# Optimization experiments

Measured on AMD Instinct MI355X. Metric: run time of the kernel, lower is better.

## Reference

```python
import jax, jax.numpy as jnp
import numpy as np

B, H, L, D = 2, 16, 1024, 64
LMAX = 2048  # max_sequence_length: patterns built & normalized at LMAX, then sliced to L
PI = float(np.pi)


def _scale_pattern(freq):
    # pattern[h, t, d] = exp(i(t+ph)) + exp(i(2t+ph)) + exp(i(0.5t+ph)), ph = 2*pi*h/H
    # identical across d, so keep [H, L, 1] and broadcast over D
    phase = 2.0 * PI * jnp.arange(H, dtype=jnp.float32) / H          # [H]
    t = jnp.linspace(0.0, 2.0 * PI * freq, LMAX)                     # [LMAX]
    a1 = t[None, :] + phase[:, None]
    a2 = 2.0 * t[None, :] + phase[:, None]
    a3 = 0.5 * t[None, :] + phase[:, None]
    pr = jnp.cos(a1) + jnp.cos(a2) + jnp.cos(a3)                     # [H, LMAX]
    pi_ = jnp.sin(a1) + jnp.sin(a2) + jnp.sin(a3)
    norm = jnp.sqrt(jnp.sum(pr * pr + pi_ * pi_, axis=1, keepdims=True))  # over full LMAX
    pr, pi_ = pr / norm, pi_ / norm
    return pr[:, :L, None], pi_[:, :L, None]                          # [H, L, 1]


def _expert_total_pattern():
    # 8 experts x 3 aspects; pattern[t, d] = exp(i(f*t + 2*pi*d/D)), normalized per
    # column over LMAX (|exp|=1 -> norm sqrt(LMAX)). Elementwise complex multiply is
    # linear, so the expert stage equals x * sum(all patterns)/(sqrt(3)*sqrt(8)).
    freqs = np.array([[0.3 + 0.1 * i, 0.2 + 0.1 * i, 0.1 + 0.1 * i]
                      for i in range(8)], dtype=np.float32).reshape(-1)   # [24]
    t = jnp.linspace(0.0, 2.0 * PI, LMAX)                                 # [LMAX]
    phase_d = 2.0 * PI * jnp.arange(D, dtype=jnp.float32) / D             # [D]
    ang = jnp.asarray(freqs)[:, None, None] * t[None, :, None] + phase_d[None, None, :]  # [24, LMAX, D]
    col_norm = 1.0 / np.sqrt(float(LMAX))
    denom = np.sqrt(3.0) * np.sqrt(8.0)
    pr = jnp.sum(jnp.cos(ang), axis=0) * (col_norm / denom)               # [LMAX, D]
    pi_ = jnp.sum(jnp.sin(ang), axis=0) * (col_norm / denom)
    return pr[:L], pi_[:L]                                                # [L, D]


def _process_scale(Qr, Qi, Kr, Ki, Vr, Vi, pr, pi_):
    # complex elementwise pattern multiply
    Qpr = Qr * pr - Qi * pi_
    Qpi = Qr * pi_ + Qi * pr
    Kpr = Kr * pr - Ki * pi_
    Kpi = Kr * pi_ + Ki * pr
    # complex scores = Qp @ Kp^T (no conjugation, matching the torch code)
    sr = jnp.einsum('bhld,bhmd->bhlm', Qpr, Kpr) - jnp.einsum('bhld,bhmd->bhlm', Qpi, Kpi)
    si = jnp.einsum('bhld,bhmd->bhlm', Qpr, Kpi) + jnp.einsum('bhld,bhmd->bhlm', Qpi, Kpr)
    mag = jnp.sqrt(sr * sr + si * si) / np.sqrt(float(D))
    w = jax.nn.softmax(mag, axis=-1)
    return (jnp.einsum('bhlm,bhmd->bhld', w, Vr),
            jnp.einsum('bhlm,bhmd->bhld', w, Vi))


def reference(Q_real, Q_imag, K_real, K_imag, V_real, V_imag):
    scale_freqs = [1.0, 0.5, 0.25, 0.1]  # char, word, phrase, sentence
    acc_r = jnp.zeros_like(Q_real)
    acc_i = jnp.zeros_like(Q_real)
    for f in scale_freqs:
        pr, pi_ = _scale_pattern(f)
        o_r, o_i = _process_scale(Q_real, Q_imag, K_real, K_imag, V_real, V_imag, pr, pi_)
        acc_r = acc_r + o_r
        acc_i = acc_i + o_i
    inv = 1.0 / np.sqrt(float(len(scale_freqs)))
    acc_r = acc_r * inv
    acc_i = acc_i * inv
    # expert mixing (linear in x -> single fused complex elementwise multiply)
    epr, epi = _expert_total_pattern()  # [L, D], broadcast over B,H
    out_r = acc_r * epr - acc_i * epi
    out_i = acc_r * epi + acc_i * epr
    return jnp.stack([out_r, out_i], axis=0)  # [2, B, H, L, D] (real, imag)


def setup_inputs() -> dict:
    key = jax.random.key(0)
    ks = jax.random.split(key, 6)
    shape = (B, H, L, D)
    names = ['Q_real', 'Q_imag', 'K_real', 'K_imag', 'V_real', 'V_imag']
    return {n: jax.random.normal(k, shape, dtype=jnp.float32) for n, k in zip(names, ks)}
```

## Files before the change

### kernel.cpp

```cpp
#include <hip/hip_runtime.h>
#include <math.h>

typedef short bf16x8 __attribute__((ext_vector_type(8)));
typedef float f32x4 __attribute__((ext_vector_type(4)));

#define BDIM 256
constexpr int B_ = 2, H_ = 16, L_ = 1024, D_ = 64, LMAX_ = 2048;
constexpr int BH_ = B_ * H_;
constexpr float PI_F = 3.14159265358979323846f;

constexpr int WS_SVP = 0;
constexpr int WS_KBR = 65536;
constexpr int WS_KBI = WS_KBR + 1048576;
constexpr int WS_VTR = WS_KBI + 1048576;
constexpr int WS_VTI = WS_VTR + 1048576;

__device__ __forceinline__ unsigned short f2b(float x) {
    union { float f; unsigned u; } v; v.f = x;
    return (unsigned short)((v.u + 0x8000u) >> 16);
}
__device__ __forceinline__ unsigned pk2(float a, float b) {
    union { float f; unsigned u; } va, vb; va.f = a; vb.f = b;
    return ((va.u + 0x8000u) >> 16) | ((vb.u + 0x8000u) & 0xFFFF0000u);
}
__device__ __forceinline__ uint4 pack4(const float4& a, const float4& b) {
    return make_uint4(pk2(a.x, a.y), pk2(a.z, a.w), pk2(b.x, b.y), pk2(b.z, b.w));
}

#define MFMA(a, b, c) __builtin_amdgcn_mfma_f32_16x16x32_bf16((a), (b), (c), 0, 0, 0)

__device__ __forceinline__ float a_val(int s, int l, float4 invn) {
    const float fr = (s == 0) ? 1.0f : (s == 1) ? 0.5f : (s == 2) ? 0.25f : 0.1f;
    const float iv = (s == 0) ? invn.x : (s == 1) ? invn.y : (s == 2) ? invn.z : invn.w;
    float t = (2.0f * PI_F * fr / (float)(LMAX_ - 1)) * (float)l;
    float m2 = 3.0f + 2.0f * cosf(t) + 2.0f * cosf(0.5f * t) + 2.0f * cosf(1.5f * t);
    return sqrtf(fmaxf(m2, 0.0f)) * iv;
}

__global__ __launch_bounds__(BDIM)
void prep_kernel(const float* __restrict__ Kr, const float* __restrict__ Ki,
                 const float* __restrict__ Vr, const float* __restrict__ Vi,
                 float* __restrict__ ws) {
    const int tid = threadIdx.x;
    const int blk = blockIdx.x;
    unsigned short* KbR = (unsigned short*)(ws + WS_KBR);
    unsigned short* KbI = (unsigned short*)(ws + WS_KBI);
    unsigned short* VtR = (unsigned short*)(ws + WS_VTR);
    unsigned short* VtI = (unsigned short*)(ws + WS_VTI);

    if (blk < 256) {
        const int comp = blk >> 7;
        const float* src = comp ? Ki : Kr;
        unsigned short* dst = comp ? KbI : KbR;
        size_t b0 = (size_t)(blk & 127) * 16384;
#pragma unroll
        for (int i = 0; i < 4; ++i) {
            size_t e = b0 + (size_t)(i * 256 + tid) * 16;
            float4 x0 = *(const float4*)(src + e);
            float4 x1 = *(const float4*)(src + e + 4);
            float4 x2 = *(const float4*)(src + e + 8);
            float4 x3 = *(const float4*)(src + e + 12);
            *(uint4*)(dst + e) = pack4(x0, x1);
            *(uint4*)(dst + e + 8) = pack4(x2, x3);
        }
    } else {
        __shared__ unsigned short sT[64 * 70];
        __shared__ float sRed[4 * 64];
        const int vb = blk - 256;
        const int comp = vb & 1, mt = (vb >> 1) & 15, bh = vb >> 5;
        const int m0 = mt * 64;
        const float* src = (comp ? Vi : Vr) + (size_t)bh * 65536 + (size_t)m0 * 64;
        unsigned short* dstA = (comp ? VtI : VtR) + (size_t)bh * 65536;
#pragma unroll
        for (int i = 0; i < 4; ++i) {
            int e = i * 256 + tid;
            int m = e >> 4, d4 = (e & 15) * 4;
            float4 x = *(const float4*)(src + (size_t)m * 64 + d4);
            *(uint2*)&sT[m * 70 + d4] = make_uint2(pk2(x.x, x.y), pk2(x.z, x.w));
        }
        {
            int d = tid & 63, grp = tid >> 6;
            float s = 0.0f;
#pragma unroll
            for (int k = 0; k < 16; ++k) s += src[(size_t)(grp * 16 + k) * 64 + d];
            sRed[grp * 64 + d] = s;
        }
        __syncthreads();
        {
            int d = tid >> 2, ms = (tid & 3) * 16;
            unsigned short v[16];
#pragma unroll
            for (int k = 0; k < 16; ++k) v[k] = sT[(ms + k) * 70 + d];
            unsigned short* dst = dstA + (size_t)d * 1024 + m0 + ms;
            *(uint4*)dst = make_uint4((unsigned)v[0] | ((unsigned)v[1] << 16),
                                      (unsigned)v[2] | ((unsigned)v[3] << 16),
                                      (unsigned)v[4] | ((unsigned)v[5] << 16),
                                      (unsigned)v[6] | ((unsigned)v[7] << 16));
            *(uint4*)(dst + 8) = make_uint4((unsigned)v[8] | ((unsigned)v[9] << 16),
                                            (unsigned)v[10] | ((unsigned)v[11] << 16),
                                            (unsigned)v[12] | ((unsigned)v[13] << 16),
                                            (unsigned)v[14] | ((unsigned)v[15] << 16));
        }
        if (tid < 64)
            ws[WS_SVP + comp * 32768 + bh * 1024 + mt * 64 + tid] =
                sRed[tid] + sRed[64 + tid] + sRed[128 + tid] + sRed[192 + tid];
    }
}

__device__ __forceinline__ void stage64s(const unsigned short* g0, int stride,
                                         unsigned short* lds, int w, int lane) {
#pragma unroll
    for (int i = 0; i < 2; ++i) {
        int c = w * 2 + i;
        int lrow = c * 8 + (lane >> 3);
        int lg = (lane & 7) ^ (lrow & 7);
        const unsigned short* src = g0 + (size_t)lrow * stride + lg * 8;
        __builtin_amdgcn_global_load_lds(
            (const __attribute__((address_space(1))) void*)src,
            (__attribute__((address_space(3))) void*)(lds + c * 512), 16, 0, 0);
    }
}
__device__ __forceinline__ bf16x8 ldfrag(const unsigned short* b, int row, int g) {
    return *(const bf16x8*)&b[row * 64 + ((g ^ (row & 7)) << 3)];
}

__global__ __launch_bounds__(BDIM, 2)
void attn_kernel(const float* __restrict__ Qr, const float* __restrict__ Qi,
                 const float* __restrict__ ws, float* __restrict__ out, float4 invn) {
    __shared__ unsigned short sK0[2][4096], sK1[2][4096];
    __shared__ unsigned short sV0[4096], sV1[4096];
    __shared__ unsigned short sE[4096];
    __shared__ unsigned short sMg[4096];
    __shared__ unsigned short sAmb[4 * 1032];
    __shared__ float sDen[4 * 64];

    const int tid = threadIdx.x;
    const int lane = tid & 63;
    const int w = tid >> 6;
    const int lo16 = lane & 15;
    const int quad = lane >> 4;
    const int blk = blockIdx.x;
    const int bh = (blk & 7) * 4 + (blk >> 7);
    const int qt = (blk >> 3) & 15;
    const int l0 = qt * 64;
    const size_t base = (size_t)bh * (L_ * D_);

    const unsigned short* gKr = (const unsigned short*)(ws + WS_KBR) + (size_t)bh * 65536;
    const unsigned short* gKi = (const unsigned short*)(ws + WS_KBI) + (size_t)bh * 65536;
    const unsigned short* gVr = (const unsigned short*)(ws + WS_VTR) + (size_t)bh * 65536;
    const unsigned short* gVi = (const unsigned short*)(ws + WS_VTI) + (size_t)bh * 65536;

    stage64s(gKr, 64, sK0[0], w, lane);
    stage64s(gKi, 64, sK1[0], w, lane);

    for (int e = tid; e < 4096; e += BDIM) {
        int s = e >> 10, l = e & 1023;
        sAmb[s * 1032 + l] = f2b(a_val(s, l, invn) * 0.125f);
    }

    bf16x8 fQr0, fQr1, fQi0, fQi1, fnQi0, fnQi1;
    {
        const int ql = l0 + w * 16 + lo16;
        const float* qr = Qr + base + (size_t)ql * 64;
        const float* qi = Qi + base + (size_t)ql * 64;
        float4 a0 = *(const float4*)(qr + quad * 8);
        float4 a1 = *(const float4*)(qr + quad * 8 + 4);
        float4 b0 = *(const float4*)(qr + 32 + quad * 8);
        float4 b1 = *(const float4*)(qr + 32 + quad * 8 + 4);
        *(uint4*)&fQr0 = pack4(a0, a1);
        *(uint4*)&fQr1 = pack4(b0, b1);
        a0 = *(const float4*)(qi + quad * 8);
        a1 = *(const float4*)(qi + quad * 8 + 4);
        b0 = *(const float4*)(qi + 32 + quad * 8);
        b1 = *(const float4*)(qi + 32 + quad * 8 + 4);
        *(uint4*)&fQi0 = pack4(a0, a1);
        *(uint4*)&fQi1 = pack4(b0, b1);
        uint4 t0 = *(uint4*)&fQi0, t1 = *(uint4*)&fQi1;
        t0.x ^= 0x80008000u; t0.y ^= 0x80008000u; t0.z ^= 0x80008000u; t0.w ^= 0x80008000u;
        t1.x ^= 0x80008000u; t1.y ^= 0x80008000u; t1.z ^= 0x80008000u; t1.w ^= 0x80008000u;
        *(uint4*)&fnQi0 = t0; *(uint4*)&fnQi1 = t1;
    }

    bf16x8 uf1a = (bf16x8){0, 0, 0, 0, 0, 0, 0, 0};
    uf1a[0] = (short)f2b(a_val(quad, l0 + w * 16 + lo16, invn) * (1.0f / 1024.0f));

    f32x4 accM1 = (f32x4){0.f, 0.f, 0.f, 0.f};
    f32x4 aOutR[4], aOutI[4];
#pragma unroll
    for (int dt = 0; dt < 4; ++dt) {
        aOutR[dt] = (f32x4){0.f, 0.f, 0.f, 0.f};
        aOutI[dt] = (f32x4){0.f, 0.f, 0.f, 0.f};
    }

    __syncthreads();

    int cur = 0;
#pragma unroll 1
    for (int mt = 0; mt < 16; ++mt) {
        const int m0 = mt * 64;
        stage64s(gVr + m0, 1024, sV0, w, lane);
        stage64s(gVi + m0, 1024, sV1, w, lane);
        if (mt < 15) {
            stage64s(gKr + (size_t)(m0 + 64) * 64, 64, sK0[cur ^ 1], w, lane);
            stage64s(gKi + (size_t)(m0 + 64) * 64, 64, sK1[cur ^ 1], w, lane);
        }
        const unsigned short* cK0 = sK0[cur];
        const unsigned short* cK1 = sK1[cur];

#pragma unroll
        for (int ct = 0; ct < 4; ++ct) {
            const int mrow = ct * 16 + lo16;
            bf16x8 kr0 = ldfrag(cK0, mrow, quad), kr1 = ldfrag(cK0, mrow, quad + 4);
            bf16x8 ki0 = ldfrag(cK1, mrow, quad), ki1 = ldfrag(cK1, mrow, quad + 4);
            f32x4 aR = (f32x4){0.f, 0.f, 0.f, 0.f};
            f32x4 aI = (f32x4){0.f, 0.f, 0.f, 0.f};
            __builtin_amdgcn_s_setprio(1);
            aR = MFMA(kr0, fQr0, aR);  aR = MFMA(kr1, fQr1, aR);
            aR = MFMA(ki0, fnQi0, aR); aR = MFMA(ki1, fnQi1, aR);
            aI = MFMA(ki0, fQr0, aI);  aI = MFMA(ki1, fQr1, aI);
            aI = MFMA(kr0, fQi0, aI);  aI = MFMA(kr1, fQi1, aI);
            __builtin_amdgcn_s_setprio(0);
            float mg0 = sqrtf(fmaf(aR[0], aR[0], aI[0] * aI[0]));
            float mg1 = sqrtf(fmaf(aR[1], aR[1], aI[1] * aI[1]));
            float mg2 = sqrtf(fmaf(aR[2], aR[2], aI[2] * aI[2]));
            float mg3 = sqrtf(fmaf(aR[3], aR[3], aI[3] * aI[3]));
            bf16x8 bf1 = (bf16x8){0, 0, 0, 0, 0, 0, 0, 0};
            bf1[0] = (short)sAmb[quad * 1032 + m0 + ct * 16 + lo16];
            f32x4 z = (f32x4){0.f, 0.f, 0.f, 0.f};
            f32x4 a1 = MFMA(bf1, uf1a, z);
            float p0 = mg0 * a1[0], p1 = mg1 * a1[1];
            float p2 = mg2 * a1[2], p3 = mg3 * a1[3];
            int l = w * 16 + lo16;
            int gph = (ct * 2 + (quad >> 1)) ^ (l & 7);
            *(uint2*)&sE[l * 64 + gph * 8 + (quad & 1) * 4] =
                make_uint2(pk2(p0, p1), pk2(p2, p3));
            *(uint2*)&sMg[l * 64 + gph * 8 + (quad & 1) * 4] =
                make_uint2(pk2(mg0, mg1), pk2(mg2, mg3));
        }
        {
            bf16x8 mf0 = ldfrag(sMg, w * 16 + lo16, quad);
            bf16x8 mf1 = ldfrag(sMg, w * 16 + lo16, quad + 4);
            bf16x8 b0 = (bf16x8){0, 0, 0, 0, 0, 0, 0, 0};
            bf16x8 b1 = (bf16x8){0, 0, 0, 0, 0, 0, 0, 0};
            if (lo16 < 4) {
                b0 = *(const bf16x8*)&sAmb[lo16 * 1032 + m0 + quad * 8];
                b1 = *(const bf16x8*)&sAmb[lo16 * 1032 + m0 + 32 + quad * 8];
            }
            accM1 = MFMA(mf0, b0, accM1);
            accM1 = MFMA(mf1, b1, accM1);
        }
        if (mt < 15) {
            asm volatile("s_waitcnt vmcnt(4)" ::: "memory");
        } else {
            asm volatile("s_waitcnt vmcnt(0)" ::: "memory");
        }
        __builtin_amdgcn_s_barrier();
        {
            bf16x8 pa0 = ldfrag(sE, w * 16 + lo16, quad);
            bf16x8 pa1 = ldfrag(sE, w * 16 + lo16, quad + 4);
            __builtin_amdgcn_s_setprio(1);
#pragma unroll
            for (int dt = 0; dt < 4; ++dt) {
                int dr = dt * 16 + lo16;
                bf16x8 vr0 = ldfrag(sV0, dr, quad), vr1 = ldfrag(sV0, dr, quad + 4);
                bf16x8 vi0 = ldfrag(sV1, dr, quad), vi1 = ldfrag(sV1, dr, quad + 4);
                aOutR[dt] = MFMA(pa0, vr0, aOutR[dt]);
                aOutR[dt] = MFMA(pa1, vr1, aOutR[dt]);
                aOutI[dt] = MFMA(pa0, vi0, aOutI[dt]);
                aOutI[dt] = MFMA(pa1, vi1, aOutI[dt]);
            }
            __builtin_amdgcn_s_setprio(0);
        }
        asm volatile("s_waitcnt vmcnt(0)" ::: "memory");
        __builtin_amdgcn_s_barrier();
        cur ^= 1;
    }

    if (lo16 < 4) {
#pragma unroll
        for (int reg = 0; reg < 4; ++reg) {
            int r = w * 16 + quad * 4 + reg;
            float alv = a_val(lo16, l0 + r, invn);
            sDen[lo16 * 64 + r] = 1.0f / (1024.0f + alv * accM1[reg]);
        }
    }
    float cden[4];
#pragma unroll
    for (int reg = 0; reg < 4; ++reg) {
        int r = w * 16 + quad * 4 + reg;
        cden[reg] = sDen[r] + sDen[64 + r] + sDen[128 + r] + sDen[192 + r];
    }

    const float cE = rsqrtf(2048.0f) * rsqrtf(24.0f);
    float eRr[4], eRi[4];
#pragma unroll
    for (int reg = 0; reg < 4; ++reg) {
        int lrow = l0 + w * 16 + quad * 4 + reg;
        float tl = (2.0f * PI_F / (float)(LMAX_ - 1)) * (float)lrow;
        float s1, c1;
        __sincosf(0.1f * tl, &s1, &c1);
        const float W[10] = {1.f, 2.f, 3.f, 3.f, 3.f, 3.f, 3.f, 3.f, 2.f, 1.f};
        float cr = c1, ci = s1;
        float er = W[0] * cr, ei = W[0] * ci;
#pragma unroll
        for (int k = 1; k < 10; ++k) {
            float nr = cr * c1 - ci * s1;
            float ni = cr * s1 + ci * c1;
            cr = nr; ci = ni;
            er = fmaf(W[k], cr, er);
            ei = fmaf(W[k], ci, ei);
        }
        eRr[reg] = er * cE;
        eRi[reg] = ei * cE;
    }

    const size_t ooff = (size_t)BH_ * L_ * D_;
#pragma unroll
    for (int dt = 0; dt < 4; ++dt) {
        int d = dt * 16 + lo16;
        float svr = 0.0f, svi = 0.0f;
#pragma unroll
        for (int q = 0; q < 16; ++q) {
            svr += ws[WS_SVP + bh * 1024 + q * 64 + d];
            svi += ws[WS_SVP + 32768 + bh * 1024 + q * 64 + d];
        }
        float sp, cp;
        __sincosf((2.0f * PI_F / 64.0f) * (float)d, &sp, &cp);
#pragma unroll
        for (int reg = 0; reg < 4; ++reg) {
            int lrow = l0 + w * 16 + quad * 4 + reg;
            float numR = fmaf(cden[reg], svr, aOutR[dt][reg]) * 0.5f;
            float numI = fmaf(cden[reg], svi, aOutI[dt][reg]) * 0.5f;
            float epr = cp * eRr[reg] - sp * eRi[reg];
            float epi = sp * eRr[reg] + cp * eRi[reg];
            size_t o = base + (size_t)lrow * 64 + d;
            out[o] = numR * epr - numI * epi;
            out[o + ooff] = numR * epi + numI * epr;
        }
    }
}

extern "C" void kernel_launch(void* const* d_in, const int* in_sizes, int n_in,
                              void* d_out, int out_size, void* d_ws, size_t ws_size,
                              hipStream_t stream) {
    const float* Qr = (const float*)d_in[0];
    const float* Qi = (const float*)d_in[1];
    const float* Kr = (const float*)d_in[2];
    const float* Ki = (const float*)d_in[3];
    const float* Vr = (const float*)d_in[4];
    const float* Vi = (const float*)d_in[5];
    float* ws = (float*)d_ws;
    float* out = (float*)d_out;

    const double fr[4] = {1.0, 0.5, 0.25, 0.1};
    float inv[4];
    for (int s = 0; s < 4; ++s) {
        double a = 2.0 * 3.14159265358979323846 * fr[s] / (double)(LMAX_ - 1);
        double S = 3.0 * LMAX_;
        const double mul[3] = {1.0, 0.5, 1.5};
        for (int k = 0; k < 3; ++k) {
            double x = a * mul[k];
            S += 2.0 * (cos(x * 1023.5) * sin(x * 1024.0) / sin(x * 0.5));
        }
        inv[s] = (float)(1.0 / sqrt(S));
    }
    float4 invn = make_float4(inv[0], inv[1], inv[2], inv[3]);

    prep_kernel<<<1280, BDIM, 0, stream>>>(Kr, Ki, Vr, Vi, ws);
    attn_kernel<<<512, BDIM, 0, stream>>>(Qr, Qi, ws, out, invn);
}
```

Measured before the change: 152.2 us.

## Use hardware bf16 pack and sqrt, reuse staged amplitudes, vectorize partial-sum reads

Several micro-optimizations land together. Software bf16 rounding is replaced with the v_cvt_pk_bf16_f32 instruction and sqrtf with raw v_sqrt_f32. The per-row amplitude is now read from the shared-memory table sAmb instead of being recomputed with cosf calls, which needs the barrier moved earlier. The prep kernel writes partial sums transposed so the epilogue can read them with float4 loads instead of 32 strided scalar loads. Raw v_sqrt_f32 drops the precise sqrt correction sequence, and the amplitude now comes from bf16-stored values rather than fp32, so precision may shift slightly.

```diff
diff --git a/kernel.cpp b/kernel.cpp
--- a/kernel.cpp
+++ b/kernel.cpp
@@ -19,12 +19,26 @@
     union { float f; unsigned u; } v; v.f = x;
     return (unsigned short)((v.u + 0x8000u) >> 16);
 }
+__device__ __forceinline__ float b2f(unsigned short x) {
+    union { unsigned u; float f; } v; v.u = ((unsigned)x) << 16;
+    return v.f;
+}
 __device__ __forceinline__ unsigned pk2(float a, float b) {
     union { float f; unsigned u; } va, vb; va.f = a; vb.f = b;
     return ((va.u + 0x8000u) >> 16) | ((vb.u + 0x8000u) & 0xFFFF0000u);
 }
 __device__ __forceinline__ uint4 pack4(const float4& a, const float4& b) {
     return make_uint4(pk2(a.x, a.y), pk2(a.z, a.w), pk2(b.x, b.y), pk2(b.z, b.w));
+}
+__device__ __forceinline__ unsigned cvtpk(float lo, float hi) {
+    unsigned r;
+    asm("v_cvt_pk_bf16_f32 %0, %1, %2" : "=v"(r) : "v"(lo), "v"(hi));
+    return r;
+}
+__device__ __forceinline__ float vsqrt(float x) {
+    float r;
+    asm("v_sqrt_f32 %0, %1" : "=v"(r) : "v"(x));
+    return r;
 }
 
 #define MFMA(a, b, c) __builtin_amdgcn_mfma_f32_16x16x32_bf16((a), (b), (c), 0, 0, 0)
@@ -102,7 +116,7 @@
                                             (unsigned)v[14] | ((unsigned)v[15] << 16));
         }
         if (tid < 64)
-            ws[WS_SVP + comp * 32768 + bh * 1024 + mt * 64 + tid] =
+            ws[WS_SVP + comp * 32768 + bh * 1024 + tid * 16 + mt] =
                 sRed[tid] + sRed[64 + tid] + sRed[128 + tid] + sRed[192 + tid];
     }
 }
@@ -181,8 +195,11 @@
         *(uint4*)&fnQi0 = t0; *(uint4*)&fnQi1 = t1;
     }
 
+    __syncthreads();
+
     bf16x8 uf1a = (bf16x8){0, 0, 0, 0, 0, 0, 0, 0};
-    uf1a[0] = (short)f2b(a_val(quad, l0 + w * 16 + lo16, invn) * (1.0f / 1024.0f));
+    uf1a[0] = (short)f2b(b2f(sAmb[quad * 1032 + (l0 + w * 16 + lo16)]) *
+                         (1.0f / 128.0f));
 
     f32x4 accM1 = (f32x4){0.f, 0.f, 0.f, 0.f};
     f32x4 aOutR[4], aOutI[4];
@@ -192,12 +209,10 @@
         aOutI[dt] = (f32x4){0.f, 0.f, 0.f, 0.f};
     }
 
-    __syncthreads();
-
-    int cur = 0;
 #pragma unroll 1
     for (int mt = 0; mt < 16; ++mt) {
         const int m0 = mt * 64;
+        const int cur = mt & 1;
         stage64s(gVr + m0, 1024, sV0, w, lane);
         stage64s(gVi + m0, 1024, sV1, w, lane);
         if (mt < 15) {
@@ -220,10 +235,10 @@
             aI = MFMA(ki0, fQr0, aI);  aI = MFMA(ki1, fQr1, aI);
             aI = MFMA(kr0, fQi0, aI);  aI = MFMA(kr1, fQi1, aI);
             __builtin_amdgcn_s_setprio(0);
-            float mg0 = sqrtf(fmaf(aR[0], aR[0], aI[0] * aI[0]));
-            float mg1 = sqrtf(fmaf(aR[1], aR[1], aI[1] * aI[1]));
-            float mg2 = sqrtf(fmaf(aR[2], aR[2], aI[2] * aI[2]));
-            float mg3 = sqrtf(fmaf(aR[3], aR[3], aI[3] * aI[3]));
+            float mg0 = vsqrt(fmaf(aR[0], aR[0], aI[0] * aI[0]));
+            float mg1 = vsqrt(fmaf(aR[1], aR[1], aI[1] * aI[1]));
+            float mg2 = vsqrt(fmaf(aR[2], aR[2], aI[2] * aI[2]));
+            float mg3 = vsqrt(fmaf(aR[3], aR[3], aI[3] * aI[3]));
             bf16x8 bf1 = (bf16x8){0, 0, 0, 0, 0, 0, 0, 0};
             bf1[0] = (short)sAmb[quad * 1032 + m0 + ct * 16 + lo16];
             f32x4 z = (f32x4){0.f, 0.f, 0.f, 0.f};
@@ -233,9 +248,9 @@
             int l = w * 16 + lo16;
             int gph = (ct * 2 + (quad >> 1)) ^ (l & 7);
             *(uint2*)&sE[l * 64 + gph * 8 + (quad & 1) * 4] =
-                make_uint2(pk2(p0, p1), pk2(p2, p3));
+                make_uint2(cvtpk(p0, p1), cvtpk(p2, p3));
             *(uint2*)&sMg[l * 64 + gph * 8 + (quad & 1) * 4] =
-                make_uint2(pk2(mg0, mg1), pk2(mg2, mg3));
+                make_uint2(cvtpk(mg0, mg1), cvtpk(mg2, mg3));
         }
         {
             bf16x8 mf0 = ldfrag(sMg, w * 16 + lo16, quad);
@@ -273,14 +288,13 @@
         }
         asm volatile("s_waitcnt vmcnt(0)" ::: "memory");
         __builtin_amdgcn_s_barrier();
-        cur ^= 1;
     }
 
     if (lo16 < 4) {
 #pragma unroll
         for (int reg = 0; reg < 4; ++reg) {
             int r = w * 16 + quad * 4 + reg;
-            float alv = a_val(lo16, l0 + r, invn);
+            float alv = b2f(sAmb[lo16 * 1032 + (l0 + r)]) * 8.0f;
             sDen[lo16 * 64 + r] = 1.0f / (1024.0f + alv * accM1[reg]);
         }
     }
@@ -318,12 +332,20 @@
 #pragma unroll
     for (int dt = 0; dt < 4; ++dt) {
         int d = dt * 16 + lo16;
-        float svr = 0.0f, svi = 0.0f;
-#pragma unroll
-        for (int q = 0; q < 16; ++q) {
-            svr += ws[WS_SVP + bh * 1024 + q * 64 + d];
-            svi += ws[WS_SVP + 32768 + bh * 1024 + q * 64 + d];
-        }
+        const float* svp = ws + WS_SVP + bh * 1024 + (size_t)d * 16;
+        float4 r0 = *(const float4*)(svp);
+        float4 r1 = *(const float4*)(svp + 4);
+        float4 r2 = *(const float4*)(svp + 8);
+        float4 r3 = *(const float4*)(svp + 12);
+        float svr = (r0.x + r0.y + r0.z + r0.w) + (r1.x + r1.y + r1.z + r1.w) +
+                    (r2.x + r2.y + r2.z + r2.w) + (r3.x + r3.y + r3.z + r3.w);
+        const float* svq = svp + 32768;
+        r0 = *(const float4*)(svq);
+        r1 = *(const float4*)(svq + 4);
+        r2 = *(const float4*)(svq + 8);
+        r3 = *(const float4*)(svq + 12);
+        float svi = (r0.x + r0.y + r0.z + r0.w) + (r1.x + r1.y + r1.z + r1.w) +
+                    (r2.x + r2.y + r2.z + r2.w) + (r3.x + r3.y + r3.z + r3.w);
         float sp, cp;
         __sincosf((2.0f * PI_F / 64.0f) * (float)d, &sp, &cp);
 #pragma unroll
```

New measurement: 143.8 us. 5.5% less time.
